# Kernel optimization log

Hardware: AMD Instinct MI355X
Metric: run time of the kernel (lower is better)

The kernel has to match this reference:

```python
import jax, jax.numpy as jnp
import numpy as np

L = 16            # n_levels
F = 2             # n_features_per_level
T = 2 ** 20       # hashmap size (power of 2)
N_MIN = 16.0
SCALE = 1.26
PI1 = np.uint32(1)
PI2 = np.uint32(2654435761)
N_PTS = 2097152


def setup_inputs() -> dict:
    key = jax.random.key(0)
    k1, k2 = jax.random.split(key)
    x = jax.random.uniform(k1, (N_PTS, 2), dtype=jnp.float32)
    # torch.rand(T,F,L)*2e-4 - 1e-4
    hash_table = jax.random.uniform(k2, (T, F, L), dtype=jnp.float32) * 0.0002 - 0.0001
    return {"x": x, "hash_table": hash_table}


def _hash(ix, iy):
    # torch does int64 xor then % T; since T=2^20 divides 2^32 and coords are
    # nonnegative, uint32 wraparound arithmetic gives identical low bits.
    return (jnp.bitwise_xor(ix * PI1, iy * PI2) % jnp.uint32(T)).astype(jnp.int32)


def _encode(x, hash_table):
    n = x.shape[0]
    # per-level resolutions, floor(N_min * b^l), computed in fp32 like torch
    NL = jnp.floor(N_MIN * jnp.power(jnp.float32(SCALE), jnp.arange(L, dtype=jnp.float32)))  # [L]
    xNL = x[:, :, None] * NL                      # [N, 2, L]
    xi = xNL.astype(jnp.int32)                    # trunc == floor for x >= 0
    local = xNL - xi.astype(xNL.dtype)            # [N, 2, L]
    ix = xi[:, 0, :].astype(jnp.uint32)           # [N, L]
    iy = xi[:, 1, :].astype(jnp.uint32)
    h0 = _hash(ix, iy)
    h1 = _hash(ix + 1, iy)
    h2 = _hash(ix, iy + 1)
    h3 = _hash(ix + 1, iy + 1)
    # hash_table[T,F,L] -> [L,T,F] so we can gather per (level, hash) pair
    Ht = jnp.transpose(hash_table, (2, 0, 1))     # [L, T, F]
    lev = jnp.broadcast_to(jnp.arange(L), h0.shape)  # [N, L]
    H0 = Ht[lev, h0]                              # [N, L, F]
    H1 = Ht[lev, h1]
    H2 = Ht[lev, h2]
    H3 = Ht[lev, h3]
    x1 = local[:, 0, :][:, :, None]               # [N, L, 1]
    x2 = local[:, 1, :][:, :, None]
    y = ((1 - x1) * (1 - x2) * H0 + x1 * (1 - x2) * H1
         + (1 - x1) * x2 * H2 + x1 * x2 * H3)     # [N, L, F]
    return y.reshape(n, L * F)


def reference(x, hash_table):
    return _encode(x, hash_table)
```

## Files before the change

### kernel.cpp

```cpp
#include <hip/hip_runtime.h>

#define NLEVELS 16
#define TMASK 0xFFFFFu
#define PI2 2654435761u
#define DENSE_TOTAL 711664u
#define NBUCK 4096
#define NPARTS 256

typedef float vfloat4 __attribute__((ext_vector_type(4)));

__constant__ float c_NL[NLEVELS] = {
    16.f, 20.f, 25.f, 32.f, 40.f, 50.f, 64.f, 80.f,
    101.f, 128.f, 161.f, 203.f, 256.f, 322.f, 406.f, 512.f
};

__device__ __forceinline__ unsigned bf16rn(float f) {
    unsigned u = __float_as_uint(f);
    return (u + 0x7FFFu + ((u >> 16) & 1u)) >> 16;
}

__global__ __launch_bounds__(256) void dense_build_kernel(
    const float* __restrict__ tb, unsigned* __restrict__ dense)
{
    constexpr unsigned kOFF[16] = {0u,289u,730u,1406u,2495u,4176u,6777u,11002u,
        17563u,27967u,44608u,70852u,112468u,178517u,282846u,448495u};
    constexpr unsigned kW[16] = {17u,21u,26u,33u,41u,51u,65u,81u,
        102u,129u,162u,204u,257u,323u,407u,513u};

    unsigned e = blockIdx.x * 256u + threadIdx.x;
    if (e >= DENSE_TOTAL) return;

    unsigned off = 0u, w = 17u; int l = 0;
    #pragma unroll
    for (int k = 1; k < 16; ++k) {
        if (e >= kOFF[k]) { off = kOFF[k]; w = kW[k]; l = k; }
    }
    unsigned rem = e - off;
    unsigned cy = rem / w;
    unsigned cx = rem - cy * w;

    unsigned h = (cx ^ (cy * PI2)) & TMASK;
    float f0 = tb[(size_t)h * 32 + l];
    float f1 = tb[(size_t)h * 32 + 16 + l];
    dense[e] = bf16rn(f0) | (bf16rn(f1) << 16);
}

__global__ __launch_bounds__(256) void hist_part_kernel(
    const float2* __restrict__ x, int* __restrict__ h, int npts, int chunk)
{
    __shared__ int sh[NBUCK];
    for (int i = threadIdx.x; i < NBUCK; i += 256) sh[i] = 0;
    __syncthreads();
    int b = blockIdx.x;
    int start = b * chunk;
    int end = min(npts, start + chunk);
    for (int i = start + (int)threadIdx.x; i < end; i += 256) {
        float2 p = x[i];
        int bx = min(63, (int)(p.x * 64.f));
        int by = min(63, (int)(p.y * 64.f));
        atomicAdd(&sh[by * 64 + bx], 1);
    }
    __syncthreads();
    int* hb = h + (size_t)b * NBUCK;
    for (int i = threadIdx.x; i < NBUCK; i += 256) hb[i] = sh[i];
}

__global__ __launch_bounds__(256) void binsum_kernel(
    const int* __restrict__ h, int* __restrict__ tot)
{
    int bin = blockIdx.x * 256 + threadIdx.x;
    int acc = 0;
    for (int b = 0; b < NPARTS; ++b) acc += h[(size_t)b * NBUCK + bin];
    tot[bin] = acc;
}

__global__ __launch_bounds__(1024) void scan_kernel(
    const int* __restrict__ tot, int* __restrict__ base)
{
    __shared__ int s[1024];
    int t = threadIdx.x;
    int v[4], pre[4], sum = 0;
    #pragma unroll
    for (int j = 0; j < 4; ++j) {
        v[j] = tot[t * 4 + j];
        pre[j] = sum;
        sum += v[j];
    }
    s[t] = sum;
    __syncthreads();
    for (int d = 1; d < 1024; d <<= 1) {
        int a = (t >= d) ? s[t - d] : 0;
        __syncthreads();
        s[t] += a;
        __syncthreads();
    }
    int bb = s[t] - sum;
    #pragma unroll
    for (int j = 0; j < 4; ++j)
        base[t * 4 + j] = bb + pre[j];
}

__global__ __launch_bounds__(256) void binoff_kernel(
    const int* __restrict__ h, const int* __restrict__ base,
    int* __restrict__ off)
{
    int bin = blockIdx.x * 256 + threadIdx.x;
    int acc = base[bin];
    for (int b = 0; b < NPARTS; ++b) {
        off[(size_t)b * NBUCK + bin] = acc;
        acc += h[(size_t)b * NBUCK + bin];
    }
}

__global__ __launch_bounds__(256) void scatter_part_kernel(
    const float2* __restrict__ x, const int* __restrict__ off,
    float2* __restrict__ xs, int* __restrict__ idx, int npts, int chunk)
{
    __shared__ int cnt[NBUCK];
    int b = blockIdx.x;
    const int* ob = off + (size_t)b * NBUCK;
    for (int i = threadIdx.x; i < NBUCK; i += 256) cnt[i] = ob[i];
    __syncthreads();
    int start = b * chunk;
    int end = min(npts, start + chunk);
    for (int i = start + (int)threadIdx.x; i < end; i += 256) {
        float2 p = x[i];
        int bx = min(63, (int)(p.x * 64.f));
        int by = min(63, (int)(p.y * 64.f));
        int pos = atomicAdd(&cnt[by * 64 + bx], 1);
        xs[pos] = p;
        idx[pos] = i;
    }
}

__global__ __launch_bounds__(256) void encode_sorted_dense_kernel(
    const float2* __restrict__ xs, const int* __restrict__ idx,
    const unsigned* __restrict__ dense, vfloat4* __restrict__ out, int npts)
{
    constexpr unsigned kOFF[16] = {0u,289u,730u,1406u,2495u,4176u,6777u,11002u,
        17563u,27967u,44608u,70852u,112468u,178517u,282846u,448495u};
    constexpr int kW[16] = {17,21,26,33,41,51,65,81,102,129,162,204,257,323,407,513};

    __shared__ vfloat4 stg[256 * 9];
    __shared__ int soi[256];

    int i = blockIdx.x * 256 + threadIdx.x;
    vfloat4 res[8];
    int oi = -1;
    if (i < npts) {
        float2 p = xs[i];
        oi = idx[i];
        #pragma unroll
        for (int g = 0; g < 2; ++g) {
            unsigned Hu[8][4];
            float lxv[8], lyv[8];
            #pragma unroll
            for (int k = 0; k < 8; ++k) {
                const int l = g * 8 + k;
                float nl = c_NL[l];
                float fx = p.x * nl;
                float fy = p.y * nl;
                int ix = (int)fx;
                int iy = (int)fy;
                lxv[k] = fx - (float)ix;
                lyv[k] = fy - (float)iy;
                const unsigned* grid = dense + kOFF[l];
                int b = iy * kW[l] + ix;
                Hu[k][0] = grid[b];
                Hu[k][1] = grid[b + 1];
                Hu[k][2] = grid[b + kW[l]];
                Hu[k][3] = grid[b + kW[l] + 1];
            }
            #pragma unroll
            for (int k = 0; k < 8; k += 2) {
                float r[4];
                #pragma unroll
                for (int m = 0; m < 2; ++m) {
                    float lx = lxv[k + m], ly = lyv[k + m];
                    float w0 = (1.f - lx) * (1.f - ly);
                    float w1 = lx * (1.f - ly);
                    float w2 = (1.f - lx) * ly;
                    float w3 = lx * ly;
                    unsigned u0 = Hu[k + m][0], u1 = Hu[k + m][1];
                    unsigned u2 = Hu[k + m][2], u3 = Hu[k + m][3];
                    float a0 = __uint_as_float(u0 << 16), b0 = __uint_as_float(u0 & 0xFFFF0000u);
                    float a1 = __uint_as_float(u1 << 16), b1 = __uint_as_float(u1 & 0xFFFF0000u);
                    float a2 = __uint_as_float(u2 << 16), b2 = __uint_as_float(u2 & 0xFFFF0000u);
                    float a3 = __uint_as_float(u3 << 16), b3 = __uint_as_float(u3 & 0xFFFF0000u);
                    r[2*m]   = w0*a0 + w1*a1 + w2*a2 + w3*a3;
                    r[2*m+1] = w0*b0 + w1*b1 + w2*b2 + w3*b3;
                }
                vfloat4 v; v.x = r[0]; v.y = r[1]; v.z = r[2]; v.w = r[3];
                res[g * 4 + (k >> 1)] = v;
            }
        }
    } else {
        #pragma unroll
        for (int k = 0; k < 8; ++k) res[k] = (vfloat4)(0.f);
    }

    soi[threadIdx.x] = oi;
    #pragma unroll
    for (int k = 0; k < 8; ++k) stg[threadIdx.x * 9 + k] = res[k];
    __syncthreads();

    int r0 = threadIdx.x >> 3;
    int j  = threadIdx.x & 7;
    #pragma unroll
    for (int p = 0; p < 8; ++p) {
        int row = p * 32 + r0;
        int o = soi[row];
        if (o >= 0)
            __builtin_nontemporal_store(stg[row * 9 + j], out + (size_t)o * 8 + j);
    }
}

__global__ __launch_bounds__(256) void hashgrid_kernel(
    const float2* __restrict__ x, const float* __restrict__ tb,
    float2* __restrict__ out, int npts)
{
    int tid = blockIdx.x * blockDim.x + threadIdx.x;
    int n = tid >> 4;
    int l = tid & 15;
    if (n >= npts) return;

    float2 xy = x[n];
    float nl = c_NL[l];
    float fx = xy.x * nl;
    float fy = xy.y * nl;
    int ixi = (int)fx;
    int iyi = (int)fy;
    float lx = fx - (float)ixi;
    float ly = fy - (float)iyi;
    unsigned ix = (unsigned)ixi, iy = (unsigned)iyi;

    unsigned hy0 = iy * PI2;
    unsigned hy1 = (iy + 1u) * PI2;
    unsigned h0 = (ix        ^ hy0) & TMASK;
    unsigned h1 = ((ix + 1u) ^ hy0) & TMASK;
    unsigned h2 = (ix        ^ hy1) & TMASK;
    unsigned h3 = ((ix + 1u) ^ hy1) & TMASK;

    const float* p0 = tb + ((size_t)h0 * 32 + l);
    const float* p1 = tb + ((size_t)h1 * 32 + l);
    const float* p2 = tb + ((size_t)h2 * 32 + l);
    const float* p3 = tb + ((size_t)h3 * 32 + l);
    float a0 = p0[0], b0 = p0[16];
    float a1 = p1[0], b1 = p1[16];
    float a2 = p2[0], b2 = p2[16];
    float a3 = p3[0], b3 = p3[16];

    float w0 = (1.f - lx) * (1.f - ly);
    float w1 = lx * (1.f - ly);
    float w2 = (1.f - lx) * ly;
    float w3 = lx * ly;
    float o0 = w0 * a0 + w1 * a1 + w2 * a2 + w3 * a3;
    float o1 = w0 * b0 + w1 * b1 + w2 * b2 + w3 * b3;

    out[(size_t)n * NLEVELS + l] = make_float2(o0, o1);
}

extern "C" void kernel_launch(void* const* d_in, const int* in_sizes, int n_in,
                              void* d_out, int out_size, void* d_ws, size_t ws_size,
                              hipStream_t stream) {
    const float2* x = (const float2*)d_in[0];
    const float* tb = (const float*)d_in[1];
    int npts = in_sizes[0] / 2;

    size_t dense_bytes = ((size_t)DENSE_TOTAL * 4 + 255) & ~(size_t)255;
    size_t xs_off      = dense_bytes;
    size_t xs_bytes    = ((size_t)npts * 8 + 255) & ~(size_t)255;
    size_t idx_off     = xs_off + xs_bytes;
    size_t idx_bytes   = ((size_t)npts * 4 + 255) & ~(size_t)255;
    size_t h_off       = idx_off + idx_bytes;
    size_t h_bytes     = (size_t)NPARTS * NBUCK * 4;
    size_t tot_off     = h_off + h_bytes;
    size_t tot_bytes   = NBUCK * 4;
    size_t base_off    = tot_off + tot_bytes;
    size_t off_off     = base_off + tot_bytes;
    size_t need        = off_off + h_bytes;

    if (ws_size >= need) {
        char* ws = (char*)d_ws;
        unsigned* dense = (unsigned*)ws;
        float2* xs    = (float2*)(ws + xs_off);
        int* idx      = (int*)(ws + idx_off);
        int* h        = (int*)(ws + h_off);
        int* tot      = (int*)(ws + tot_off);
        int* base     = (int*)(ws + base_off);
        int* off      = (int*)(ws + off_off);

        int chunk = (npts + NPARTS - 1) / NPARTS;
        int nblk = (npts + 255) / 256;
        int dblk = (DENSE_TOTAL + 255) / 256;

        dense_build_kernel<<<dblk, 256, 0, stream>>>(tb, dense);
        hist_part_kernel<<<NPARTS, 256, 0, stream>>>(x, h, npts, chunk);
        binsum_kernel<<<NBUCK / 256, 256, 0, stream>>>(h, tot);
        scan_kernel<<<1, 1024, 0, stream>>>(tot, base);
        binoff_kernel<<<NBUCK / 256, 256, 0, stream>>>(h, base, off);
        scatter_part_kernel<<<NPARTS, 256, 0, stream>>>(x, off, xs, idx, npts, chunk);
        encode_sorted_dense_kernel<<<nblk, 256, 0, stream>>>(
            xs, idx, dense, (vfloat4*)d_out, npts);
    } else {
        long long total = (long long)npts * NLEVELS;
        long long grid = (total + 255) / 256;
        hashgrid_kernel<<<(int)grid, 256, 0, stream>>>(x, tb, (float2*)d_out, npts);
    }
}
```

Baseline: 160.5 us.

## Fuse dense build with histogram, pack sorted points with index, pair corner loads

Merges the dense-grid build and the per-partition histogram into one launch by giving each role its own range of block IDs, which removes one kernel launch and lets the two run concurrently. The sorted point coordinates and original index are packed into a single 16-byte record, so the scatter does one store and the encoder one load per point, at the cost of extra padding bytes. Adjacent corner entries of the dense grid are fetched as 8-byte pairs to halve the number of gather instructions, though those 8-byte loads may be misaligned.

```diff
diff --git a/kernel.cpp b/kernel.cpp
--- a/kernel.cpp
+++ b/kernel.cpp
@@ -4,6 +4,7 @@
 #define TMASK 0xFFFFFu
 #define PI2 2654435761u
 #define DENSE_TOTAL 711664u
+#define DBLK 2780
 #define NBUCK 4096
 #define NPARTS 256
 
@@ -19,50 +20,45 @@
     return (u + 0x7FFFu + ((u >> 16) & 1u)) >> 16;
 }
 
-__global__ __launch_bounds__(256) void dense_build_kernel(
-    const float* __restrict__ tb, unsigned* __restrict__ dense)
-{
-    constexpr unsigned kOFF[16] = {0u,289u,730u,1406u,2495u,4176u,6777u,11002u,
-        17563u,27967u,44608u,70852u,112468u,178517u,282846u,448495u};
-    constexpr unsigned kW[16] = {17u,21u,26u,33u,41u,51u,65u,81u,
-        102u,129u,162u,204u,257u,323u,407u,513u};
-
-    unsigned e = blockIdx.x * 256u + threadIdx.x;
-    if (e >= DENSE_TOTAL) return;
-
-    unsigned off = 0u, w = 17u; int l = 0;
-    #pragma unroll
-    for (int k = 1; k < 16; ++k) {
-        if (e >= kOFF[k]) { off = kOFF[k]; w = kW[k]; l = k; }
-    }
-    unsigned rem = e - off;
-    unsigned cy = rem / w;
-    unsigned cx = rem - cy * w;
-
-    unsigned h = (cx ^ (cy * PI2)) & TMASK;
-    float f0 = tb[(size_t)h * 32 + l];
-    float f1 = tb[(size_t)h * 32 + 16 + l];
-    dense[e] = bf16rn(f0) | (bf16rn(f1) << 16);
-}
-
-__global__ __launch_bounds__(256) void hist_part_kernel(
+__global__ __launch_bounds__(256) void build_hist_kernel(
+    const float* __restrict__ tb, unsigned* __restrict__ dense,
     const float2* __restrict__ x, int* __restrict__ h, int npts, int chunk)
 {
     __shared__ int sh[NBUCK];
-    for (int i = threadIdx.x; i < NBUCK; i += 256) sh[i] = 0;
-    __syncthreads();
-    int b = blockIdx.x;
-    int start = b * chunk;
-    int end = min(npts, start + chunk);
-    for (int i = start + (int)threadIdx.x; i < end; i += 256) {
-        float2 p = x[i];
-        int bx = min(63, (int)(p.x * 64.f));
-        int by = min(63, (int)(p.y * 64.f));
-        atomicAdd(&sh[by * 64 + bx], 1);
-    }
-    __syncthreads();
-    int* hb = h + (size_t)b * NBUCK;
-    for (int i = threadIdx.x; i < NBUCK; i += 256) hb[i] = sh[i];
+    if (blockIdx.x < DBLK) {
+        constexpr unsigned kOFF[16] = {0u,289u,730u,1406u,2495u,4176u,6777u,11002u,
+            17563u,27967u,44608u,70852u,112468u,178517u,282846u,448495u};
+        constexpr unsigned kW[16] = {17u,21u,26u,33u,41u,51u,65u,81u,
+            102u,129u,162u,204u,257u,323u,407u,513u};
+        unsigned e = blockIdx.x * 256u + threadIdx.x;
+        if (e >= DENSE_TOTAL) return;
+        unsigned off = 0u, w = 17u; int l = 0;
+        #pragma unroll
+        for (int k = 1; k < 16; ++k)
+            if (e >= kOFF[k]) { off = kOFF[k]; w = kW[k]; l = k; }
+        unsigned rem = e - off;
+        unsigned cy = rem / w;
+        unsigned cx = rem - cy * w;
+        unsigned hh = (cx ^ (cy * PI2)) & TMASK;
+        float f0 = tb[(size_t)hh * 32 + l];
+        float f1 = tb[(size_t)hh * 32 + 16 + l];
+        dense[e] = bf16rn(f0) | (bf16rn(f1) << 16);
+    } else {
+        for (int i = threadIdx.x; i < NBUCK; i += 256) sh[i] = 0;
+        __syncthreads();
+        int b = blockIdx.x - DBLK;
+        int start = b * chunk;
+        int end = min(npts, start + chunk);
+        for (int i = start + (int)threadIdx.x; i < end; i += 256) {
+            float2 p = x[i];
+            int bx = min(63, (int)(p.x * 64.f));
+            int by = min(63, (int)(p.y * 64.f));
+            atomicAdd(&sh[by * 64 + bx], 1);
+        }
+        __syncthreads();
+        int* hb = h + (size_t)b * NBUCK;
+        for (int i = threadIdx.x; i < NBUCK; i += 256) hb[i] = sh[i];
+    }
 }
 
 __global__ __launch_bounds__(256) void binsum_kernel(
@@ -114,7 +110,7 @@
 
 __global__ __launch_bounds__(256) void scatter_part_kernel(
     const float2* __restrict__ x, const int* __restrict__ off,
-    float2* __restrict__ xs, int* __restrict__ idx, int npts, int chunk)
+    uint4* __restrict__ xsidx, int npts, int chunk)
 {
     __shared__ int cnt[NBUCK];
     int b = blockIdx.x;
@@ -128,14 +124,14 @@
         int bx = min(63, (int)(p.x * 64.f));
         int by = min(63, (int)(p.y * 64.f));
         int pos = atomicAdd(&cnt[by * 64 + bx], 1);
-        xs[pos] = p;
-        idx[pos] = i;
+        xsidx[pos] = make_uint4(__float_as_uint(p.x), __float_as_uint(p.y),
+                                (unsigned)i, 0u);
     }
 }
 
 __global__ __launch_bounds__(256) void encode_sorted_dense_kernel(
-    const float2* __restrict__ xs, const int* __restrict__ idx,
-    const unsigned* __restrict__ dense, vfloat4* __restrict__ out, int npts)
+    const uint4* __restrict__ xsidx, const unsigned* __restrict__ dense,
+    vfloat4* __restrict__ out, int npts)
 {
     constexpr unsigned kOFF[16] = {0u,289u,730u,1406u,2495u,4176u,6777u,11002u,
         17563u,27967u,44608u,70852u,112468u,178517u,282846u,448495u};
@@ -148,11 +144,12 @@
     vfloat4 res[8];
     int oi = -1;
     if (i < npts) {
-        float2 p = xs[i];
-        oi = idx[i];
+        uint4 rec = xsidx[i];
+        float2 p = make_float2(__uint_as_float(rec.x), __uint_as_float(rec.y));
+        oi = (int)rec.z;
         #pragma unroll
         for (int g = 0; g < 2; ++g) {
-            unsigned Hu[8][4];
+            unsigned long long Hlo[8], Hhi[8];
             float lxv[8], lyv[8];
             #pragma unroll
             for (int k = 0; k < 8; ++k) {
@@ -166,10 +163,8 @@
                 lyv[k] = fy - (float)iy;
                 const unsigned* grid = dense + kOFF[l];
                 int b = iy * kW[l] + ix;
-                Hu[k][0] = grid[b];
-                Hu[k][1] = grid[b + 1];
-                Hu[k][2] = grid[b + kW[l]];
-                Hu[k][3] = grid[b + kW[l] + 1];
+                __builtin_memcpy(&Hlo[k], grid + b, 8);
+                __builtin_memcpy(&Hhi[k], grid + b + kW[l], 8);
             }
             #pragma unroll
             for (int k = 0; k < 8; k += 2) {
@@ -181,8 +176,10 @@
                     float w1 = lx * (1.f - ly);
                     float w2 = (1.f - lx) * ly;
                     float w3 = lx * ly;
-                    unsigned u0 = Hu[k + m][0], u1 = Hu[k + m][1];
-                    unsigned u2 = Hu[k + m][2], u3 = Hu[k + m][3];
+                    unsigned u0 = (unsigned)Hlo[k + m];
+                    unsigned u1 = (unsigned)(Hlo[k + m] >> 32);
+                    unsigned u2 = (unsigned)Hhi[k + m];
+                    unsigned u3 = (unsigned)(Hhi[k + m] >> 32);
                     float a0 = __uint_as_float(u0 << 16), b0 = __uint_as_float(u0 & 0xFFFF0000u);
                     float a1 = __uint_as_float(u1 << 16), b1 = __uint_as_float(u1 & 0xFFFF0000u);
                     float a2 = __uint_as_float(u2 << 16), b2 = __uint_as_float(u2 & 0xFFFF0000u);
@@ -268,11 +265,9 @@
     int npts = in_sizes[0] / 2;
 
     size_t dense_bytes = ((size_t)DENSE_TOTAL * 4 + 255) & ~(size_t)255;
-    size_t xs_off      = dense_bytes;
-    size_t xs_bytes    = ((size_t)npts * 8 + 255) & ~(size_t)255;
-    size_t idx_off     = xs_off + xs_bytes;
-    size_t idx_bytes   = ((size_t)npts * 4 + 255) & ~(size_t)255;
-    size_t h_off       = idx_off + idx_bytes;
+    size_t xsidx_off   = dense_bytes;
+    size_t xsidx_bytes = ((size_t)npts * 16 + 255) & ~(size_t)255;
+    size_t h_off       = xsidx_off + xsidx_bytes;
     size_t h_bytes     = (size_t)NPARTS * NBUCK * 4;
     size_t tot_off     = h_off + h_bytes;
     size_t tot_bytes   = NBUCK * 4;
@@ -283,8 +278,7 @@
     if (ws_size >= need) {
         char* ws = (char*)d_ws;
         unsigned* dense = (unsigned*)ws;
-        float2* xs    = (float2*)(ws + xs_off);
-        int* idx      = (int*)(ws + idx_off);
+        uint4* xsidx  = (uint4*)(ws + xsidx_off);
         int* h        = (int*)(ws + h_off);
         int* tot      = (int*)(ws + tot_off);
         int* base     = (int*)(ws + base_off);
@@ -292,16 +286,14 @@
 
         int chunk = (npts + NPARTS - 1) / NPARTS;
         int nblk = (npts + 255) / 256;
-        int dblk = (DENSE_TOTAL + 255) / 256;
-
-        dense_build_kernel<<<dblk, 256, 0, stream>>>(tb, dense);
-        hist_part_kernel<<<NPARTS, 256, 0, stream>>>(x, h, npts, chunk);
+
+        build_hist_kernel<<<DBLK + NPARTS, 256, 0, stream>>>(tb, dense, x, h, npts, chunk);
         binsum_kernel<<<NBUCK / 256, 256, 0, stream>>>(h, tot);
         scan_kernel<<<1, 1024, 0, stream>>>(tot, base);
         binoff_kernel<<<NBUCK / 256, 256, 0, stream>>>(h, base, off);
-        scatter_part_kernel<<<NPARTS, 256, 0, stream>>>(x, off, xs, idx, npts, chunk);
+        scatter_part_kernel<<<NPARTS, 256, 0, stream>>>(x, off, xsidx, npts, chunk);
         encode_sorted_dense_kernel<<<nblk, 256, 0, stream>>>(
-            xs, idx, dense, (vfloat4*)d_out, npts);
+            xsidx, dense, (vfloat4*)d_out, npts);
     } else {
         long long total = (long long)npts * NLEVELS;
         long long grid = (total + 255) / 256;
```

Result: faster. 134.7 us (-16.1%).
